# Performance work log

Measured on AMD Instinct MI355X. Metric: run time of the kernel, lower is better.

The kernel has to match this reference:

```python
import jax, jax.numpy as jnp
import numpy as np
from jax import lax

DIM = 1024
BATCH = 16
WIDTH = 2048
DECAY = 0.99


def setup_inputs() -> dict:
    key = jax.random.key(0)
    k1, k2, k3, k4 = jax.random.split(key, 4)
    scale = 1.0 / np.sqrt(DIM)
    x = jax.random.normal(k1, (BATCH, WIDTH, DIM), dtype=jnp.float32)
    state = jnp.zeros((BATCH, DIM), dtype=jnp.float32)
    Wv = jax.random.normal(k2, (DIM, DIM), dtype=jnp.float32) * scale
    Wr = jax.random.normal(k3, (DIM, DIM), dtype=jnp.float32) * scale
    Wc = jax.random.normal(k4, (DIM, DIM), dtype=jnp.float32) * scale
    return {"x": x, "state": state, "Wv": Wv, "Wr": Wr, "Wc": Wc}


def reference(x, state, Wv, Wr, Wc):
    # x: [B, W, D], state: [B, D]; fixed-decay RWKV recurrence along width.
    decay = jnp.asarray(DECAY, dtype=x.dtype)
    one_minus = jnp.asarray(1.0, dtype=x.dtype) - decay
    v = jnp.einsum('bwd,de->bwe', x, Wv)                 # value projection
    r = jax.nn.sigmoid(jnp.einsum('bwd,de->bwe', x, Wr))  # receptance

    # scan over width (time) axis: elems shaped [W, B, D]
    def step(s_prev, inp):
        v_t, r_t, x_t = inp
        s_curr = decay * s_prev + one_minus * v_t
        y_t = x_t + r_t * s_curr
        return s_curr, y_t

    elems = (jnp.swapaxes(v, 0, 1), jnp.swapaxes(r, 0, 1), jnp.swapaxes(x, 0, 1))
    new_state, y_t = lax.scan(step, state, elems)
    y = jnp.swapaxes(y_t, 0, 1)                          # [B, W, D]
    y = y + jnp.einsum('bwd,de->bwe', y, Wc)             # minimal channel mix
    return y, new_state
```

## Files before the change

### kernel.cpp

```cpp
#include <hip/hip_runtime.h>
#include <hip/hip_bf16.h>
#include <math.h>


#define MROWS 32768
#define NCHUNK 16
#define CHUNKL 128
#define DECAY_F 0.99f
#define OM_F 0.01f

typedef __attribute__((ext_vector_type(8))) short short8;
typedef __attribute__((ext_vector_type(4))) float floatx4;

using bf16 = __hip_bfloat16;
using bf162 = __hip_bfloat162;

__device__ __forceinline__ void async_copy16(const void* g, void* l) {
  __builtin_amdgcn_global_load_lds(
      (const __attribute__((address_space(1))) unsigned int*)g,
      (__attribute__((address_space(3))) unsigned int*)l, 16, 0, 0);
}

#define S_BARRIER() asm volatile("s_barrier" ::: "memory")
#define VMCNT2()                                                               \
  do {                                                                         \
    asm volatile("s_waitcnt vmcnt(2)" ::: "memory");                           \
    __builtin_amdgcn_sched_barrier(0);                                         \
  } while (0)
#define VMCNT0()                                                               \
  do {                                                                         \
    asm volatile("s_waitcnt vmcnt(0)" ::: "memory");                           \
    __builtin_amdgcn_sched_barrier(0);                                         \
  } while (0)

__global__ void prep_x(const float* __restrict__ X, bf16* __restrict__ Xb) {
  const int idx = blockIdx.x * 256 + threadIdx.x;
  const float4 v = ((const float4*)X)[idx];
  union { ushort4 u; bf16 h[4]; } pk;
  pk.h[0] = __float2bfloat16(v.x);
  pk.h[1] = __float2bfloat16(v.y);
  pk.h[2] = __float2bfloat16(v.z);
  pk.h[3] = __float2bfloat16(v.w);
  ((ushort4*)Xb)[idx] = pk.u;
}

__global__ void prep_weights(const float* __restrict__ Wv,
                             const float* __restrict__ Wr,
                             const float* __restrict__ Wc,
                             bf16* __restrict__ WT) {
  __shared__ float tile[32][33];
  const int bk = blockIdx.x * 32;
  const int bn = blockIdx.y * 32;
  const float* src;
  int nbase = bn;
  if (bn < 1024)      { src = Wv; }
  else if (bn < 2048) { src = Wr; nbase = bn - 1024; }
  else                { src = Wc; nbase = bn - 2048; }
  const int tx = threadIdx.x;
  const int ty = threadIdx.y;
  #pragma unroll
  for (int i = ty; i < 32; i += 8)
    tile[i][tx] = src[(size_t)(bk + i) * 1024 + nbase + tx];
  __syncthreads();
  #pragma unroll
  for (int i = ty; i < 32; i += 8)
    WT[(size_t)(bn + i) * 1024 + bk + tx] = __float2bfloat16(tile[tx][i]);
}

#define PH_MFMA4(M0)                                                           \
  __builtin_amdgcn_s_setprio(1);                                               \
  _Pragma("unroll")                                                            \
  for (int mf = M0; mf < M0 + 4; ++mf)                                         \
    _Pragma("unroll")                                                          \
    for (int nf = 0; nf < 4; ++nf)                                             \
      acc[mf][nf] = __builtin_amdgcn_mfma_f32_16x16x32_bf16(                   \
          fa[mf], fb[nf], acc[mf][nf], 0, 0, 0);                               \
  __builtin_amdgcn_s_setprio(0);

#define MFMA_ALL()                                                             \
  __builtin_amdgcn_s_setprio(1);                                               \
  _Pragma("unroll")                                                            \
  for (int mf = 0; mf < 8; ++mf)                                               \
    _Pragma("unroll")                                                          \
    for (int nf = 0; nf < 4; ++nf)                                             \
      acc[mf][nf] = __builtin_amdgcn_mfma_f32_16x16x32_bf16(                   \
          fa[mf], fb[nf], acc[mf][nf], 0, 0, 0);                               \
  __builtin_amdgcn_s_setprio(0);

template <int MODE>
__global__ __launch_bounds__(512, 2) void gemm8(const bf16* __restrict__ Ab,
                                                const bf16* __restrict__ Bw,
                                                bf16* __restrict__ Vout,
                                                bf16* __restrict__ Rout,
                                                float* __restrict__ Fout) {
  __shared__ char lds[65536];
  constexpr int NTN = (MODE == 0) ? 8 : 4;

  const int nwg = gridDim.x;
  const int id = blockIdx.x;
  const int wg = (id & 7) * (nwg >> 3) + (id >> 3);
  const int mt = wg / NTN, nt = wg % NTN;
  const int m0 = mt * 256, n0 = nt * 256;

  const int t = threadIdx.x;
  const int l = t & 63, w = t >> 6;
  const int wm = w >> 2, wn = w & 3;

  const int srow = w * 16 + (l >> 2);
  const int scol = ((l & 3) ^ ((l >> 3) & 3)) << 4;
  const char* Abase = (const char*)Ab;
  const char* Bbase = (const char*)Bw;
  const char* gA0 = Abase + (size_t)(m0 + srow) * 2048 + scol;
  const char* gA1 = gA0 + (size_t)128 * 2048;
  const char* gB0 = Bbase + (size_t)(n0 + srow) * 2048 + scol;
  const char* gB1 = gB0 + (size_t)128 * 2048;

  const int wb = w * 1024;

  const int ll = l & 15;
  const int laneoff = ((ll * 64) + ((l >> 4) << 4)) ^ (((ll >> 1) & 3) << 4);

  floatx4 acc[8][4];
  #pragma unroll
  for (int i = 0; i < 8; ++i)
    #pragma unroll
    for (int j = 0; j < 4; ++j) acc[i][j] = (floatx4){0.f, 0.f, 0.f, 0.f};

  async_copy16(gA0, lds + 0 + wb);
  async_copy16(gA1, lds + 8192 + wb);
  async_copy16(gB0, lds + 16384 + wb);
  async_copy16(gB1, lds + 24576 + wb);
  async_copy16(gB0 + 64, lds + 32768 + 16384 + wb);
  async_copy16(gB1 + 64, lds + 32768 + 24576 + wb);
  gA0 += 64; gA1 += 64; gB0 += 128; gB1 += 128;
  VMCNT2();
  S_BARRIER();

  short8 fa[8], fb[4];

  for (int T = 0; T < 30; ++T) {
    const int cb = (T & 1) << 15;
    const char* smA = lds + cb + wm * 8192 + laneoff;
    const char* smB = lds + cb + 16384 + wn * 4096 + laneoff;
    async_copy16(gA0, lds + (cb ^ 32768) + 0 + wb); gA0 += 64;
    async_copy16(gA1, lds + (cb ^ 32768) + 8192 + wb); gA1 += 64;
    #pragma unroll
    for (int nf = 0; nf < 4; ++nf) fb[nf] = *(const short8*)(smB + nf * 1024);
    #pragma unroll
    for (int mf = 0; mf < 8; ++mf) fa[mf] = *(const short8*)(smA + mf * 1024);
    PH_MFMA4(0)
    S_BARRIER();
    async_copy16(gB0, lds + cb + 16384 + wb); gB0 += 64;
    async_copy16(gB1, lds + cb + 24576 + wb); gB1 += 64;
    PH_MFMA4(4)
    VMCNT2();
    S_BARRIER();
  }

  {
    const char* smA = lds + wm * 8192 + laneoff;
    const char* smB = lds + 16384 + wn * 4096 + laneoff;
    #pragma unroll
    for (int nf = 0; nf < 4; ++nf) fb[nf] = *(const short8*)(smB + nf * 1024);
    #pragma unroll
    for (int mf = 0; mf < 8; ++mf) fa[mf] = *(const short8*)(smA + mf * 1024);
    async_copy16(gA0, lds + 32768 + 0 + wb);
    async_copy16(gA1, lds + 32768 + 8192 + wb);
    MFMA_ALL()
    VMCNT0();
    S_BARRIER();
  }
  {
    const char* smA = lds + 32768 + wm * 8192 + laneoff;
    const char* smB = lds + 32768 + 16384 + wn * 4096 + laneoff;
    #pragma unroll
    for (int nf = 0; nf < 4; ++nf) fb[nf] = *(const short8*)(smB + nf * 1024);
    #pragma unroll
    for (int mf = 0; mf < 8; ++mf) fa[mf] = *(const short8*)(smA + mf * 1024);
    MFMA_ALL()
  }

  const int orow0 = m0 + wm * 128 + (l >> 4) * 4;
  const int ocol = n0 + wn * 64 + ll;
  if constexpr (MODE == 0) {
    const bool isr = (n0 >= 1024);
    bf16* outp = isr ? Rout : Vout;
    const int oc = isr ? (ocol - 1024) : ocol;
    #pragma unroll
    for (int mf = 0; mf < 8; ++mf) {
      #pragma unroll
      for (int i = 0; i < 4; ++i) {
        const size_t ro = (size_t)(orow0 + mf * 16 + i) * 1024 + oc;
        #pragma unroll
        for (int nf = 0; nf < 4; ++nf) {
          float cv = acc[mf][nf][i];
          if (isr) cv = 1.0f / (1.0f + __expf(-cv));
          outp[ro + nf * 16] = __float2bfloat16(cv);
        }
      }
    }
  } else {
    #pragma unroll
    for (int mf = 0; mf < 8; ++mf) {
      #pragma unroll
      for (int i = 0; i < 4; ++i) {
        const size_t ro = (size_t)(orow0 + mf * 16 + i) * 1024 + ocol;
        #pragma unroll
        for (int nf = 0; nf < 4; ++nf) {
          const size_t o = ro + nf * 16;
          Fout[o] = __bfloat162float(Ab[o]) + acc[mf][nf][i];
        }
      }
    }
  }
}

__global__ void scan_partial(const bf16* __restrict__ V, float* __restrict__ sl) {
  const int idx = blockIdx.x * 256 + threadIdx.x;
  const int d2 = idx & 511;
  const int c = (idx >> 9) & 15;
  const int b = idx >> 13;
  const bf162* V2 = (const bf162*)V;
  const size_t base = (size_t)(b * 2048 + c * 128) * 512 + d2;
  float s0 = 0.f, s1 = 0.f;
  for (int w = 0; w < CHUNKL; ++w) {
    const bf162 v = V2[base + (size_t)w * 512];
    s0 = DECAY_F * s0 + OM_F * __bfloat162float(v.x);
    s1 = DECAY_F * s1 + OM_F * __bfloat162float(v.y);
  }
  const int o = (b * 16 + c) * 1024 + d2 * 2;
  sl[o] = s0;
  sl[o + 1] = s1;
}

__global__ void scan_chunk(const float* __restrict__ state,
                           const float* __restrict__ sl,
                           float* __restrict__ sin_,
                           float* __restrict__ state_out,
                           float decayL) {
  const int idx = blockIdx.x * 256 + threadIdx.x;
  const int d = idx & 1023;
  const int b = idx >> 10;
  float s = state[idx];
  #pragma unroll
  for (int c = 0; c < NCHUNK; ++c) {
    const int o = (b * 16 + c) * 1024 + d;
    sin_[o] = s;
    s = decayL * s + sl[o];
  }
  state_out[idx] = s;
}

__global__ void scan_apply(const bf16* __restrict__ Xb,
                           const bf16* __restrict__ R,
                           const float* __restrict__ sin_,
                           bf16* __restrict__ VY) {
  const int idx = blockIdx.x * 256 + threadIdx.x;
  const int d2 = idx & 511;
  const int c = (idx >> 9) & 15;
  const int b = idx >> 13;
  const bf162* R2 = (const bf162*)R;
  const bf162* X2 = (const bf162*)Xb;
  bf162* VY2 = (bf162*)VY;
  const size_t base = (size_t)(b * 2048 + c * 128) * 512 + d2;
  const int so = (b * 16 + c) * 1024 + d2 * 2;
  float s0 = sin_[so], s1 = sin_[so + 1];
  for (int w = 0; w < CHUNKL; ++w) {
    const size_t off = base + (size_t)w * 512;
    const bf162 v = VY2[off];
    const bf162 r = R2[off];
    const bf162 xx = X2[off];
    s0 = DECAY_F * s0 + OM_F * __bfloat162float(v.x);
    s1 = DECAY_F * s1 + OM_F * __bfloat162float(v.y);
    const float y0 = __bfloat162float(xx.x) + __bfloat162float(r.x) * s0;
    const float y1 = __bfloat162float(xx.y) + __bfloat162float(r.y) * s1;
    bf162 o;
    o.x = __float2bfloat16(y0);
    o.y = __float2bfloat16(y1);
    VY2[off] = o;
  }
}

extern "C" void kernel_launch(void* const* d_in, const int* in_sizes, int n_in,
                              void* d_out, int out_size, void* d_ws, size_t ws_size,
                              hipStream_t stream) {
  const float* x     = (const float*)d_in[0];
  const float* state = (const float*)d_in[1];
  const float* Wv    = (const float*)d_in[2];
  const float* Wr    = (const float*)d_in[3];
  const float* Wc    = (const float*)d_in[4];

  float* y_out = (float*)d_out;
  float* state_out = y_out + (size_t)MROWS * 1024;

  char* ws = (char*)d_ws;
  bf16* WT   = (bf16*)ws;
  bf16* Xb   = (bf16*)(ws + ((size_t)6 << 20));
  bf16* Vbuf = (bf16*)(ws + ((size_t)70 << 20));
  bf16* Rbuf = (bf16*)(ws + ((size_t)134 << 20));
  float* sl  = (float*)(ws + ((size_t)198 << 20));
  float* sin_ = (float*)(ws + ((size_t)199 << 20));
  bf16* WcT = WT + (size_t)2048 * 1024;

  const float decayL = (float)pow(0.99, (double)CHUNKL);

  prep_x<<<32768, 256, 0, stream>>>(x, Xb);
  prep_weights<<<dim3(32, 96), dim3(32, 8), 0, stream>>>(Wv, Wr, Wc, WT);
  gemm8<0><<<1024, 512, 0, stream>>>(Xb, WT, Vbuf, Rbuf, nullptr);
  scan_partial<<<512, 256, 0, stream>>>(Vbuf, sl);
  scan_chunk<<<64, 256, 0, stream>>>(state, sl, sin_, state_out, decayL);
  scan_apply<<<512, 256, 0, stream>>>(Xb, Rbuf, sin_, Vbuf);
  gemm8<1><<<512, 512, 0, stream>>>(Vbuf, WcT, nullptr, nullptr, y_out);
}
```

Baseline: 507.0 us.

## Rework bf16 GEMM mainloop with 128-wide K tiles and finer-grained staging

```diff
diff --git a/kernel.cpp b/kernel.cpp
--- a/kernel.cpp
+++ b/kernel.cpp
@@ -22,14 +22,19 @@
 }
 
 #define S_BARRIER() asm volatile("s_barrier" ::: "memory")
-#define VMCNT2()                                                               \
+#define VMCNT6()                                                               \
   do {                                                                         \
-    asm volatile("s_waitcnt vmcnt(2)" ::: "memory");                           \
+    asm volatile("s_waitcnt vmcnt(6)" ::: "memory");                           \
     __builtin_amdgcn_sched_barrier(0);                                         \
   } while (0)
 #define VMCNT0()                                                               \
   do {                                                                         \
     asm volatile("s_waitcnt vmcnt(0)" ::: "memory");                           \
+    __builtin_amdgcn_sched_barrier(0);                                         \
+  } while (0)
+#define LGKM0()                                                                \
+  do {                                                                         \
+    asm volatile("s_waitcnt lgkmcnt(0)" ::: "memory");                         \
     __builtin_amdgcn_sched_barrier(0);                                         \
   } while (0)
 
@@ -67,25 +72,43 @@
     WT[(size_t)(bn + i) * 1024 + bk + tx] = __float2bfloat16(tile[tx][i]);
 }
 
-#define PH_MFMA4(M0)                                                           \
+
+#define MFMA16(MB, FA)                                                         \
   __builtin_amdgcn_s_setprio(1);                                               \
   _Pragma("unroll")                                                            \
-  for (int mf = M0; mf < M0 + 4; ++mf)                                         \
-    _Pragma("unroll")                                                          \
-    for (int nf = 0; nf < 4; ++nf)                                             \
-      acc[mf][nf] = __builtin_amdgcn_mfma_f32_16x16x32_bf16(                   \
-          fa[mf], fb[nf], acc[mf][nf], 0, 0, 0);                               \
+  for (int nf = 0; nf < 4; ++nf) {                                             \
+    acc[MB][nf] = __builtin_amdgcn_mfma_f32_16x16x32_bf16(                     \
+        FA[0][0], fb[nf][0], acc[MB][nf], 0, 0, 0);                            \
+    acc[MB + 1][nf] = __builtin_amdgcn_mfma_f32_16x16x32_bf16(                 \
+        FA[1][0], fb[nf][0], acc[MB + 1][nf], 0, 0, 0);                        \
+  }                                                                            \
+  _Pragma("unroll")                                                            \
+  for (int nf = 0; nf < 4; ++nf) {                                             \
+    acc[MB][nf] = __builtin_amdgcn_mfma_f32_16x16x32_bf16(                     \
+        FA[0][1], fb[nf][1], acc[MB][nf], 0, 0, 0);                            \
+    acc[MB + 1][nf] = __builtin_amdgcn_mfma_f32_16x16x32_bf16(                 \
+        FA[1][1], fb[nf][1], acc[MB + 1][nf], 0, 0, 0);                        \
+  }                                                                            \
   __builtin_amdgcn_s_setprio(0);
 
-#define MFMA_ALL()                                                             \
-  __builtin_amdgcn_s_setprio(1);                                               \
+#define READA(FA, MB, PTR)                                                     \
+  FA[0][0] = *(const short8*)((PTR) + (MB) * 2048 + lk0);                      \
+  FA[0][1] = *(const short8*)((PTR) + (MB) * 2048 + lk1);                      \
+  FA[1][0] = *(const short8*)((PTR) + ((MB) + 1) * 2048 + lk0);                \
+  FA[1][1] = *(const short8*)((PTR) + ((MB) + 1) * 2048 + lk1);
+
+#define READB(PTR)                                                             \
   _Pragma("unroll")                                                            \
-  for (int mf = 0; mf < 8; ++mf)                                               \
-    _Pragma("unroll")                                                          \
-    for (int nf = 0; nf < 4; ++nf)                                             \
-      acc[mf][nf] = __builtin_amdgcn_mfma_f32_16x16x32_bf16(                   \
-          fa[mf], fb[nf], acc[mf][nf], 0, 0, 0);                               \
-  __builtin_amdgcn_s_setprio(0);
+  for (int nf = 0; nf < 4; ++nf) {                                             \
+    fb[nf][0] = *(const short8*)((PTR) + nf * 2048 + lk0);                     \
+    fb[nf][1] = *(const short8*)((PTR) + nf * 2048 + lk1);                     \
+  }
+
+#define STAGE(GP, LOFF)                                                        \
+  do {                                                                         \
+    async_copy16((GP), lds + (LOFF) + wb);                                     \
+    async_copy16((GP) + (size_t)64 * 2048, lds + (LOFF) + 8192 + wb);          \
+  } while (0)
 
 template <int MODE>
 __global__ __launch_bounds__(512, 2) void gemm8(const bf16* __restrict__ Ab,
@@ -93,7 +116,7 @@
                                                 bf16* __restrict__ Vout,
                                                 bf16* __restrict__ Rout,
                                                 float* __restrict__ Fout) {
-  __shared__ char lds[65536];
+  extern __shared__ char lds[];
   constexpr int NTN = (MODE == 0) ? 8 : 4;
 
   const int nwg = gridDim.x;
@@ -105,20 +128,23 @@
   const int t = threadIdx.x;
   const int l = t & 63, w = t >> 6;
   const int wm = w >> 2, wn = w & 3;
-
-  const int srow = w * 16 + (l >> 2);
-  const int scol = ((l & 3) ^ ((l >> 3) & 3)) << 4;
-  const char* Abase = (const char*)Ab;
-  const char* Bbase = (const char*)Bw;
-  const char* gA0 = Abase + (size_t)(m0 + srow) * 2048 + scol;
+  const int wb = w * 1024;
+
+  const int sgrow = w * 8 + (l >> 3);
+  const int sgcol = ((l & 7) ^ ((l >> 3) & 7)) * 16;
+  const char* gA0 = (const char*)Ab + (size_t)(m0 + sgrow) * 2048 + sgcol;
   const char* gA1 = gA0 + (size_t)128 * 2048;
-  const char* gB0 = Bbase + (size_t)(n0 + srow) * 2048 + scol;
+  const char* gB0 = (const char*)Bw + (size_t)(n0 + sgrow) * 2048 + sgcol;
   const char* gB1 = gB0 + (size_t)128 * 2048;
 
-  const int wb = w * 1024;
-
-  const int ll = l & 15;
-  const int laneoff = ((ll * 64) + ((l >> 4) << 4)) ^ (((ll >> 1) & 3) << 4);
+  const int ll = l & 15, qd = l >> 4;
+  const int arow = ll * 128;
+  const int lk0 = ((qd ^ (ll & 7)) << 4);
+  const int lk1 = (((4 | qd) ^ (ll & 7)) << 4);
+  const char* pAP = lds + wm * 16384 + arow;
+  const char* pBP = lds + 32768 + (wn >> 1) * 16384 + (wn & 1) * 8192 + arow;
+  const char* pAQ = pAP + 65536;
+  const char* pBQ = pBP + 65536;
 
   floatx4 acc[8][4];
   #pragma unroll
@@ -126,58 +152,61 @@
     #pragma unroll
     for (int j = 0; j < 4; ++j) acc[i][j] = (floatx4){0.f, 0.f, 0.f, 0.f};
 
-  async_copy16(gA0, lds + 0 + wb);
-  async_copy16(gA1, lds + 8192 + wb);
-  async_copy16(gB0, lds + 16384 + wb);
-  async_copy16(gB1, lds + 24576 + wb);
-  async_copy16(gB0 + 64, lds + 32768 + 16384 + wb);
-  async_copy16(gB1 + 64, lds + 32768 + 24576 + wb);
-  gA0 += 64; gA1 += 64; gB0 += 128; gB1 += 128;
-  VMCNT2();
+  short8 fa01[2][2], fa23[2][2], fa45[2][2], fa67[2][2], fb[4][2];
+
+  STAGE(gB0, 32768);         gB0 += 128;
+  STAGE(gB1, 49152);         gB1 += 128;
+  STAGE(gA0, 0);             gA0 += 128;
+  STAGE(gA1, 16384);         gA1 += 128;
+  STAGE(gB0, 65536 + 32768); gB0 += 128;
+  STAGE(gB1, 65536 + 49152); gB1 += 128;
+  STAGE(gA0, 65536);         gA0 += 128;
+  VMCNT6();
   S_BARRIER();
 
-  short8 fa[8], fb[4];
-
-  for (int T = 0; T < 30; ++T) {
-    const int cb = (T & 1) << 15;
-    const char* smA = lds + cb + wm * 8192 + laneoff;
-    const char* smB = lds + cb + 16384 + wn * 4096 + laneoff;
-    async_copy16(gA0, lds + (cb ^ 32768) + 0 + wb); gA0 += 64;
-    async_copy16(gA1, lds + (cb ^ 32768) + 8192 + wb); gA1 += 64;
-    #pragma unroll
-    for (int nf = 0; nf < 4; ++nf) fb[nf] = *(const short8*)(smB + nf * 1024);
-    #pragma unroll
-    for (int mf = 0; mf < 8; ++mf) fa[mf] = *(const short8*)(smA + mf * 1024);
-    PH_MFMA4(0)
-    S_BARRIER();
-    async_copy16(gB0, lds + cb + 16384 + wb); gB0 += 64;
-    async_copy16(gB1, lds + cb + 24576 + wb); gB1 += 64;
-    PH_MFMA4(4)
-    VMCNT2();
-    S_BARRIER();
-  }
-
-  {
-    const char* smA = lds + wm * 8192 + laneoff;
-    const char* smB = lds + 16384 + wn * 4096 + laneoff;
-    #pragma unroll
-    for (int nf = 0; nf < 4; ++nf) fb[nf] = *(const short8*)(smB + nf * 1024);
-    #pragma unroll
-    for (int mf = 0; mf < 8; ++mf) fa[mf] = *(const short8*)(smA + mf * 1024);
-    async_copy16(gA0, lds + 32768 + 0 + wb);
-    async_copy16(gA1, lds + 32768 + 8192 + wb);
-    MFMA_ALL()
-    VMCNT0();
-    S_BARRIER();
-  }
-  {
-    const char* smA = lds + 32768 + wm * 8192 + laneoff;
-    const char* smB = lds + 32768 + 16384 + wn * 4096 + laneoff;
-    #pragma unroll
-    for (int nf = 0; nf < 4; ++nf) fb[nf] = *(const short8*)(smB + nf * 1024);
-    #pragma unroll
-    for (int mf = 0; mf < 8; ++mf) fa[mf] = *(const short8*)(smA + mf * 1024);
-    MFMA_ALL()
+  for (int j = 0; j < 8; ++j) {
+    const bool full = (j < 7);
+    READB(pBP);
+    READA(fa01, 0, pAP);
+    STAGE(gA1, 65536 + 16384); gA1 += 128;
+    S_BARRIER(); LGKM0();
+    MFMA16(0, fa01);
+    S_BARRIER();
+    READA(fa23, 2, pAP);
+    READA(fa45, 4, pAP);
+    if (full) { STAGE(gB0, 32768); gB0 += 128; }
+    S_BARRIER(); LGKM0();
+    MFMA16(2, fa23);
+    S_BARRIER();
+    READA(fa67, 6, pAP);
+    if (full) { STAGE(gB1, 49152); gB1 += 128; }
+    S_BARRIER(); LGKM0();
+    MFMA16(4, fa45);
+    S_BARRIER();
+    if (full) { STAGE(gA0, 0); gA0 += 128; }
+    MFMA16(6, fa67);
+    if (full) { VMCNT6(); } else { VMCNT0(); }
+    S_BARRIER();
+    READB(pBQ);
+    READA(fa01, 0, pAQ);
+    if (full) { STAGE(gA1, 16384); gA1 += 128; }
+    S_BARRIER(); LGKM0();
+    MFMA16(0, fa01);
+    S_BARRIER();
+    READA(fa23, 2, pAQ);
+    READA(fa45, 4, pAQ);
+    if (full) { STAGE(gB0, 65536 + 32768); gB0 += 128; }
+    S_BARRIER(); LGKM0();
+    MFMA16(2, fa23);
+    S_BARRIER();
+    READA(fa67, 6, pAQ);
+    if (full) { STAGE(gB1, 65536 + 49152); gB1 += 128; }
+    S_BARRIER(); LGKM0();
+    MFMA16(4, fa45);
+    S_BARRIER();
+    if (full) { STAGE(gA0, 65536); gA0 += 128; }
+    MFMA16(6, fa67);
+    if (full) { VMCNT6(); S_BARRIER(); }
   }
 
   const int orow0 = m0 + wm * 128 + (l >> 4) * 4;
@@ -304,11 +333,22 @@
 
   const float decayL = (float)pow(0.99, (double)CHUNKL);
 
+  static bool g_cfg = false;
+  if (!g_cfg) {
+    auto kf0 = gemm8<0>;
+    auto kf1 = gemm8<1>;
+    (void)hipFuncSetAttribute((const void*)kf0,
+                              hipFuncAttributeMaxDynamicSharedMemorySize, 131072);
+    (void)hipFuncSetAttribute((const void*)kf1,
+                              hipFuncAttributeMaxDynamicSharedMemorySize, 131072);
+    g_cfg = true;
+  }
+
   prep_x<<<32768, 256, 0, stream>>>(x, Xb);
   prep_weights<<<dim3(32, 96), dim3(32, 8), 0, stream>>>(Wv, Wr, Wc, WT);
-  gemm8<0><<<1024, 512, 0, stream>>>(Xb, WT, Vbuf, Rbuf, nullptr);
+  gemm8<0><<<1024, 512, 131072, stream>>>(Xb, WT, Vbuf, Rbuf, nullptr);
   scan_partial<<<512, 256, 0, stream>>>(Vbuf, sl);
   scan_chunk<<<64, 256, 0, stream>>>(state, sl, sin_, state_out, decayL);
   scan_apply<<<512, 256, 0, stream>>>(Xb, Rbuf, sin_, Vbuf);
-  gemm8<1><<<512, 512, 0, stream>>>(Vbuf, WcT, nullptr, nullptr, y_out);
-}
+  gemm8<1><<<512, 512, 131072, stream>>>(Vbuf, WcT, nullptr, nullptr, y_out);
+}
```

Measured after the change: 512.3 us. No clear change (+1.0%).
